# Optimization experiments

Measured on AMD Instinct MI355X. Metric: run time of the kernel, lower is better.

Reference implementation:

```python
import jax, jax.numpy as jnp
import numpy as np

N_RAYS = 1048576
N_SAMPLES = 64
FAR_DELTA = 1e10  # sentinel delta appended after last sample
EPS = 1e-10


def setup_inputs() -> dict:
    key = jax.random.key(0)
    k1, k2, k3 = jax.random.split(key, 3)
    sigmas = jax.random.normal(k1, (N_RAYS, N_SAMPLES), dtype=jnp.float32)
    rgbs = jax.random.uniform(k2, (N_RAYS, N_SAMPLES, 3), dtype=jnp.float32)
    # monotonically increasing z_vals per ray (near=2.0, positive strata)
    steps = jax.random.uniform(k3, (N_RAYS, N_SAMPLES), dtype=jnp.float32) * 0.05 + 0.01
    z_vals = 2.0 + jnp.cumsum(steps, axis=-1)
    return {"sigmas": sigmas, "rgbs": rgbs, "z_vals": z_vals}


def reference(sigmas, rgbs, z_vals):
    # deltas: (N, S); last delta is a huge value (opaque background)
    deltas = z_vals[:, 1:] - z_vals[:, :-1]
    deltas = jnp.concatenate(
        [deltas, jnp.full_like(deltas[:, :1], FAR_DELTA)], axis=-1)
    alphas = 1.0 - jnp.exp(-jax.nn.relu(sigmas) * deltas)          # (N, S)
    trans = 1.0 - alphas + EPS
    transmittance = jnp.concatenate(
        [jnp.ones_like(trans[:, :1]), trans], axis=-1)
    accum_trans = jnp.cumprod(transmittance, axis=-1)[:, :-1]       # (N, S)
    weights = alphas * accum_trans                                   # (N, S)
    rgb_final = jnp.sum(weights[..., None] * rgbs, axis=-2)          # (N, 3)
    depth_final = jnp.sum(weights * z_vals, axis=-1)                 # (N,)
    # white background compositing
    pix_alpha = jnp.sum(weights, axis=-1)                            # (N,)
    rgb_final = rgb_final + 1.0 - pix_alpha[:, None]
    return rgb_final, depth_final, accum_trans[:, -1]
```

## Files before the change

### kernel.cpp

```cpp
#include <hip/hip_runtime.h>

#define FARD 1e10f
#define EPSV 1e-10f

__global__ __launch_bounds__(256) void nerf_render_kernel(
    const float* __restrict__ sigmas,
    const float* __restrict__ rgbs,
    const float* __restrict__ z_vals,
    float* __restrict__ out,
    int n_rays)
{
    const int tid = blockIdx.x * blockDim.x + threadIdx.x;
    const int ray = tid >> 4;
    if (ray >= n_rays) return;
    const int l = threadIdx.x & 15;

    const float4 sg = *reinterpret_cast<const float4*>(sigmas + (size_t)ray * 64 + l * 4);
    const float4 zv = *reinterpret_cast<const float4*>(z_vals + (size_t)ray * 64 + l * 4);
    const float* rp = rgbs + (size_t)ray * 192 + l * 12;
    const float4 c0 = *reinterpret_cast<const float4*>(rp);
    const float4 c1 = *reinterpret_cast<const float4*>(rp + 4);
    const float4 c2 = *reinterpret_cast<const float4*>(rp + 8);

    const float zn = __shfl_down(zv.x, 1, 16);

    const float d0 = zv.y - zv.x;
    const float d1 = zv.z - zv.y;
    const float d2 = zv.w - zv.z;
    const float d3 = (l == 15) ? FARD : (zn - zv.w);

    const float e0 = __expf(-fmaxf(sg.x, 0.f) * d0);
    const float e1 = __expf(-fmaxf(sg.y, 0.f) * d1);
    const float e2 = __expf(-fmaxf(sg.z, 0.f) * d2);
    const float e3 = __expf(-fmaxf(sg.w, 0.f) * d3);

    const float a0 = 1.f - e0, a1 = 1.f - e1, a2 = 1.f - e2, a3 = 1.f - e3;
    const float t0 = e0 + EPSV, t1 = e1 + EPSV, t2 = e2 + EPSV, t3 = e3 + EPSV;

    float scan = t0 * t1 * t2 * t3;
    #pragma unroll
    for (int off = 1; off < 16; off <<= 1) {
        const float v = __shfl_up(scan, off, 16);
        if (l >= off) scan *= v;
    }
    float ex = __shfl_up(scan, 1, 16);
    if (l == 0) ex = 1.f;

    const float w0 = a0 * ex;
    float acc = ex * t0;
    const float w1 = a1 * acc; acc *= t1;
    const float w2 = a2 * acc; acc *= t2;
    const float w3 = a3 * acc;
    const float accT_62 = acc;

    float wsum = w0 + w1 + w2 + w3;
    float dsum = w0 * zv.x + w1 * zv.y + w2 * zv.z + w3 * zv.w;
    float rsum = w0 * c0.x + w1 * c0.w + w2 * c1.z + w3 * c2.y;
    float gsum = w0 * c0.y + w1 * c1.x + w2 * c1.w + w3 * c2.z;
    float bsum = w0 * c0.z + w1 * c1.y + w2 * c2.x + w3 * c2.w;

    #pragma unroll
    for (int off = 8; off >= 1; off >>= 1) {
        wsum += __shfl_xor(wsum, off, 16);
        dsum += __shfl_xor(dsum, off, 16);
        rsum += __shfl_xor(rsum, off, 16);
        gsum += __shfl_xor(gsum, off, 16);
        bsum += __shfl_xor(bsum, off, 16);
    }

    if (l == 0) {
        const float bg = 1.f - wsum;
        out[(size_t)ray * 3 + 0] = rsum + bg;
        out[(size_t)ray * 3 + 1] = gsum + bg;
        out[(size_t)ray * 3 + 2] = bsum + bg;
        out[(size_t)3 * n_rays + ray] = dsum;
    }
    if (l == 15) {
        out[(size_t)4 * n_rays + ray] = accT_62;
    }
}

extern "C" void kernel_launch(void* const* d_in, const int* in_sizes, int n_in,
                              void* d_out, int out_size, void* d_ws, size_t ws_size,
                              hipStream_t stream) {
    const float* sigmas = (const float*)d_in[0];
    const float* rgbs   = (const float*)d_in[1];
    const float* z_vals = (const float*)d_in[2];
    float* out = (float*)d_out;

    const int n_rays = in_sizes[0] / 64;
    const int threads = 256;
    const long long total_threads = (long long)n_rays * 16;
    const int blocks = (int)((total_threads + threads - 1) / threads);

    nerf_render_kernel<<<blocks, threads, 0, stream>>>(sigmas, rgbs, z_vals, out, n_rays);
}
```

Before: 244.1 us.

## Process eight samples per thread with local scan before cross-lane scan

Each ray is now handled by 8 lanes of 8 samples each instead of 16 lanes of 4. Each thread runs a sequential transmittance product and partial weighted sums locally. It then scales them by the exclusive cross-lane prefix, which shortens the shuffle scan and reduction chains. Output stores are spread across lanes so the RGB, depth and transmittance writes happen in parallel. The trade-off is higher register use, wider per-thread loads and fewer threads per ray on a memory-bound kernel.

After: 240.8 us. Within noise of the previous version (-1.4%).

```diff
diff --git a/kernel.cpp b/kernel.cpp
--- a/kernel.cpp
+++ b/kernel.cpp
@@ -11,72 +11,78 @@
     int n_rays)
 {
     const int tid = blockIdx.x * blockDim.x + threadIdx.x;
-    const int ray = tid >> 4;
+    const int ray = tid >> 3;
     if (ray >= n_rays) return;
-    const int l = threadIdx.x & 15;
+    const int l = threadIdx.x & 7;
 
-    const float4 sg = *reinterpret_cast<const float4*>(sigmas + (size_t)ray * 64 + l * 4);
-    const float4 zv = *reinterpret_cast<const float4*>(z_vals + (size_t)ray * 64 + l * 4);
-    const float* rp = rgbs + (size_t)ray * 192 + l * 12;
-    const float4 c0 = *reinterpret_cast<const float4*>(rp);
-    const float4 c1 = *reinterpret_cast<const float4*>(rp + 4);
-    const float4 c2 = *reinterpret_cast<const float4*>(rp + 8);
+    const float4* sp = reinterpret_cast<const float4*>(sigmas + (size_t)ray * 64 + l * 8);
+    const float4* zp = reinterpret_cast<const float4*>(z_vals + (size_t)ray * 64 + l * 8);
+    const float4* cp = reinterpret_cast<const float4*>(rgbs   + (size_t)ray * 192 + l * 24);
+    const float4 s0 = sp[0], s1 = sp[1];
+    const float4 z0 = zp[0], z1 = zp[1];
+    const float4 c0 = cp[0], c1 = cp[1], c2 = cp[2];
+    const float4 c3 = cp[3], c4 = cp[4], c5 = cp[5];
 
-    const float zn = __shfl_down(zv.x, 1, 16);
+    const float zz[8] = {z0.x, z0.y, z0.z, z0.w, z1.x, z1.y, z1.z, z1.w};
+    const float sv[8] = {s0.x, s0.y, s0.z, s0.w, s1.x, s1.y, s1.z, s1.w};
+    const float cc[24] = {c0.x, c0.y, c0.z, c0.w, c1.x, c1.y, c1.z, c1.w,
+                          c2.x, c2.y, c2.z, c2.w, c3.x, c3.y, c3.z, c3.w,
+                          c4.x, c4.y, c4.z, c4.w, c5.x, c5.y, c5.z, c5.w};
 
-    const float d0 = zv.y - zv.x;
-    const float d1 = zv.z - zv.y;
-    const float d2 = zv.w - zv.z;
-    const float d3 = (l == 15) ? FARD : (zn - zv.w);
+    const float zn = __shfl_down(z0.x, 1, 8);
 
-    const float e0 = __expf(-fmaxf(sg.x, 0.f) * d0);
-    const float e1 = __expf(-fmaxf(sg.y, 0.f) * d1);
-    const float e2 = __expf(-fmaxf(sg.z, 0.f) * d2);
-    const float e3 = __expf(-fmaxf(sg.w, 0.f) * d3);
+    float d[8];
+    #pragma unroll
+    for (int k = 0; k < 7; ++k) d[k] = zz[k + 1] - zz[k];
+    d[7] = (l == 7) ? FARD : (zn - zz[7]);
 
-    const float a0 = 1.f - e0, a1 = 1.f - e1, a2 = 1.f - e2, a3 = 1.f - e3;
-    const float t0 = e0 + EPSV, t1 = e1 + EPSV, t2 = e2 + EPSV, t3 = e3 + EPSV;
+    float run = 1.f;
+    float P6  = 1.f;
+    float Wp = 0.f, Dp = 0.f, Rp = 0.f, Gp = 0.f, Bp = 0.f;
+    #pragma unroll
+    for (int k = 0; k < 8; ++k) {
+        const float e = __expf(-fmaxf(sv[k], 0.f) * d[k]);
+        const float u = (1.f - e) * run;
+        if (k == 7) P6 = run;
+        run *= (e + EPSV);
+        Wp += u;
+        Dp += u * zz[k];
+        Rp += u * cc[3 * k + 0];
+        Gp += u * cc[3 * k + 1];
+        Bp += u * cc[3 * k + 2];
+    }
 
-    float scan = t0 * t1 * t2 * t3;
+    float scan = run;
     #pragma unroll
-    for (int off = 1; off < 16; off <<= 1) {
-        const float v = __shfl_up(scan, off, 16);
+    for (int off = 1; off < 8; off <<= 1) {
+        const float v = __shfl_up(scan, off, 8);
         if (l >= off) scan *= v;
     }
-    float ex = __shfl_up(scan, 1, 16);
+    float ex = __shfl_up(scan, 1, 8);
     if (l == 0) ex = 1.f;
 
-    const float w0 = a0 * ex;
-    float acc = ex * t0;
-    const float w1 = a1 * acc; acc *= t1;
-    const float w2 = a2 * acc; acc *= t2;
-    const float w3 = a3 * acc;
-    const float accT_62 = acc;
-
-    float wsum = w0 + w1 + w2 + w3;
-    float dsum = w0 * zv.x + w1 * zv.y + w2 * zv.z + w3 * zv.w;
-    float rsum = w0 * c0.x + w1 * c0.w + w2 * c1.z + w3 * c2.y;
-    float gsum = w0 * c0.y + w1 * c1.x + w2 * c1.w + w3 * c2.z;
-    float bsum = w0 * c0.z + w1 * c1.y + w2 * c2.x + w3 * c2.w;
-
+    float wsum = ex * Wp;
+    float dsum = ex * Dp;
+    float rsum = ex * Rp;
+    float gsum = ex * Gp;
+    float bsum = ex * Bp;
     #pragma unroll
-    for (int off = 8; off >= 1; off >>= 1) {
-        wsum += __shfl_xor(wsum, off, 16);
-        dsum += __shfl_xor(dsum, off, 16);
-        rsum += __shfl_xor(rsum, off, 16);
-        gsum += __shfl_xor(gsum, off, 16);
-        bsum += __shfl_xor(bsum, off, 16);
+    for (int off = 4; off >= 1; off >>= 1) {
+        wsum += __shfl_xor(wsum, off, 8);
+        dsum += __shfl_xor(dsum, off, 8);
+        rsum += __shfl_xor(rsum, off, 8);
+        gsum += __shfl_xor(gsum, off, 8);
+        bsum += __shfl_xor(bsum, off, 8);
     }
 
-    if (l == 0) {
-        const float bg = 1.f - wsum;
-        out[(size_t)ray * 3 + 0] = rsum + bg;
-        out[(size_t)ray * 3 + 1] = gsum + bg;
-        out[(size_t)ray * 3 + 2] = bsum + bg;
+    const float bg = 1.f - wsum;
+    if (l < 3) {
+        const float v = (l == 0) ? rsum : ((l == 1) ? gsum : bsum);
+        out[(size_t)ray * 3 + l] = v + bg;
+    } else if (l == 3) {
         out[(size_t)3 * n_rays + ray] = dsum;
-    }
-    if (l == 15) {
-        out[(size_t)4 * n_rays + ray] = accT_62;
+    } else if (l == 7) {
+        out[(size_t)4 * n_rays + ray] = ex * P6;
     }
 }
 
@@ -90,7 +96,7 @@
 
     const int n_rays = in_sizes[0] / 64;
     const int threads = 256;
-    const long long total_threads = (long long)n_rays * 16;
+    const long long total_threads = (long long)n_rays * 8;
     const int blocks = (int)((total_threads + threads - 1) / threads);
 
     nerf_render_kernel<<<blocks, threads, 0, stream>>>(sigmas, rgbs, z_vals, out, n_rays);
```
